# Kernel tuning notes

Hardware: AMD Instinct MI355X
Metric: run time of the kernel (lower is better)

## Reference

```python
import jax, jax.numpy as jnp
import numpy as np

B, T, D, A = 16, 2048, 512, 64


def setup_inputs() -> dict:
    key = jax.random.key(0)
    ks = jax.random.split(key, 7)
    s = 1.0 / np.sqrt(D)
    return {
        "inp": jax.random.normal(ks[0], (B, T, D), dtype=jnp.float32),
        "Wq": jax.random.normal(ks[1], (D, A), dtype=jnp.float32) * s,
        "bq": jax.random.normal(ks[2], (A,), dtype=jnp.float32) * 0.01,
        "Wk": jax.random.normal(ks[3], (D, A), dtype=jnp.float32) * s,
        "bk": jax.random.normal(ks[4], (A,), dtype=jnp.float32) * 0.01,
        "Wv": jax.random.normal(ks[5], (D, A), dtype=jnp.float32) * s,
        "bv": jax.random.normal(ks[6], (A,), dtype=jnp.float32) * 0.01,
    }


def reference(inp, Wq, bq, Wk, bk, Wv, bv):
    # Projections: (B,T,D) @ (D,A) -> (B,T,A)
    Q = inp @ Wq + bq
    K = inp @ Wk + bk
    V = inp @ Wv + bv
    # Scaled QK^T: (B,T,T)
    scores = jnp.einsum("btd,bsd->bts", Q, K) / jnp.sqrt(jnp.float32(A))
    # Sign-based K padding mask: mask[b, s] = sign(|sum_a K[b,s,a]|)
    k_mask = jnp.sign(jnp.abs(K.sum(axis=-1)))  # (B,T)
    scores = jnp.where(k_mask[:, None, :] == 0, jnp.float32(1e-8), scores)
    att = jax.nn.softmax(scores, axis=-1)
    # Sign-based Q mask broadcast along the key axis (faithful to Mask module)
    q_mask = jnp.sign(jnp.abs(Q.sum(axis=-1)))  # (B,T)
    att = att * q_mask[:, None, :]
    # dropout_keep_prob == 1 -> dropout is identity
    ctx = jnp.einsum("bts,bsa->bta", att, V)  # (B,T,A)
    # inp^T @ ctx -> (B,D,A), then sum over A -> (B,D)
    out = jnp.einsum("btd,bta->bd", inp, ctx)
    return out
```

## Files before the change

kernel.cpp:

```cpp
#include <hip/hip_runtime.h>

#define B_ 16
#define T_ 2048
#define D_ 512
#define SCALE_LOG2E 0.18033688f

typedef __bf16 bf16x8 __attribute__((ext_vector_type(8)));
typedef float  f32x4  __attribute__((ext_vector_type(4)));

__device__ inline unsigned short f2bf(float f){
    union { float f; unsigned u; } x; x.f = f;
    unsigned r = x.u + 0x7fffu + ((x.u >> 16) & 1u);
    return (unsigned short)(r >> 16);
}

__device__ inline bf16x8 ldfrag(const unsigned short* p){
    uint4 v = *reinterpret_cast<const uint4*>(p);
    return __builtin_bit_cast(bf16x8, v);
}


__global__ void setup_kernel(const float* __restrict__ Wq, const float* __restrict__ Wk,
                             const float* __restrict__ Wv, const float* __restrict__ bq,
                             const float* __restrict__ bk, const float* __restrict__ bv,
                             unsigned short* __restrict__ WcT, float* __restrict__ bsum,
                             float* __restrict__ numden, float* __restrict__ out)
{
    int e = blockIdx.x * 256 + threadIdx.x;
    if (e < 73728){
        int j = e >> 9, d = e & 511;
        float v;
        if (j < 64)       v = Wq[d * 64 + j];
        else if (j < 128) v = Wk[d * 64 + (j - 64)];
        else if (j < 131){
            const float* src = (j == 128) ? Wq : (j == 129) ? Wk : Wv;
            const float4* p = reinterpret_cast<const float4*>(&src[d * 64]);
            v = 0.f;
            #pragma unroll
            for (int i = 0; i < 16; i++){ float4 t = p[i]; v += (t.x + t.y) + (t.z + t.w); }
        }
        else v = 0.f;
        WcT[j * 512 + d] = f2bf(v);
    } else if (e < 73744){
        int mm = e - 73728;
        float s = 0.f;
        const float* src = (mm == 0) ? bq : (mm == 1) ? bk : bv;
        if (mm < 3){
            const float4* p = reinterpret_cast<const float4*>(src);
            #pragma unroll
            for (int i = 0; i < 16; i++){ float4 t = p[i]; s += (t.x + t.y) + (t.z + t.w); }
        }
        bsum[mm] = s;
    } else if (e < 139280){
        numden[e - 73744] = 0.f;
    } else if (e < 147472){
        out[e - 139280] = 0.f;
    }
}

__global__ __launch_bounds__(256) void proj_kernel(
    const float* __restrict__ inp, const unsigned short* __restrict__ WcT,
    const float* __restrict__ bq, const float* __restrict__ bk,
    const float* __restrict__ bsum,
    unsigned short* __restrict__ Qb, unsigned short* __restrict__ Kb,
    float* __restrict__ wvp)
{
    __shared__ __align__(16) unsigned short Af[4 * 512];
    __shared__ __align__(16) unsigned short Bf[9 * 512];
    const int tid  = threadIdx.x;
    const int r0   = blockIdx.x * 64;
    const int lane = tid & 63, wvid = tid >> 6;
    const int m = lane & 15, q = lane >> 4;

    const int ar = tid >> 2, aseg = tid & 3;
    unsigned short* a_dst = &Af[(ar >> 4) * 512 + (aseg * 16 + (ar & 15)) * 8];
    const float* a_src = &inp[(size_t)(r0 + ar) * 512 + aseg * 8];
    const unsigned short* b_src0 = &WcT[(((tid      ) >> 6) * 16 + (tid & 15)) * 512 + ((tid >> 4) & 3) * 8];
    const unsigned short* b_src1 = &WcT[(((tid + 256) >> 6) * 16 + (tid & 15)) * 512 + ((tid >> 4) & 3) * 8];
    const unsigned short* b_src2 = &WcT[(((tid + 512) >> 6) * 16 + (tid & 15)) * 512 + ((tid >> 4) & 3) * 8];
    uint4* b_dst0 = reinterpret_cast<uint4*>(&Bf[(tid      ) * 8]);
    uint4* b_dst1 = reinterpret_cast<uint4*>(&Bf[(tid + 256) * 8]);
    uint4* b_dst2 = reinterpret_cast<uint4*>(&Bf[(tid + 512) * 8]);

    f32x4 acc[9];
    #pragma unroll
    for (int t = 0; t < 9; t++) acc[t] = (f32x4){0.f, 0.f, 0.f, 0.f};

    float4 ga0 = *reinterpret_cast<const float4*>(a_src);
    float4 ga1 = *reinterpret_cast<const float4*>(a_src + 4);
    uint4 gb0 = *reinterpret_cast<const uint4*>(b_src0);
    uint4 gb1 = *reinterpret_cast<const uint4*>(b_src1);
    uint4 gb2 = (tid < 64) ? *reinterpret_cast<const uint4*>(b_src2) : (uint4){0,0,0,0};

    for (int kk = 0; kk < 512; kk += 32){
        uint4 pk;
        pk.x = f2bf(ga0.x) | ((unsigned)f2bf(ga0.y) << 16);
        pk.y = f2bf(ga0.z) | ((unsigned)f2bf(ga0.w) << 16);
        pk.z = f2bf(ga1.x) | ((unsigned)f2bf(ga1.y) << 16);
        pk.w = f2bf(ga1.z) | ((unsigned)f2bf(ga1.w) << 16);
        *reinterpret_cast<uint4*>(a_dst) = pk;
        *b_dst0 = gb0;
        *b_dst1 = gb1;
        if (tid < 64) *b_dst2 = gb2;
        __syncthreads();
        if (kk < 480){
            ga0 = *reinterpret_cast<const float4*>(a_src + kk + 32);
            ga1 = *reinterpret_cast<const float4*>(a_src + kk + 36);
            gb0 = *reinterpret_cast<const uint4*>(b_src0 + kk + 32);
            gb1 = *reinterpret_cast<const uint4*>(b_src1 + kk + 32);
            if (tid < 64) gb2 = *reinterpret_cast<const uint4*>(b_src2 + kk + 32);
        }
        bf16x8 a = ldfrag(&Af[wvid * 512 + lane * 8]);
        #pragma unroll
        for (int t = 0; t < 9; t++){
            bf16x8 bfr = ldfrag(&Bf[t * 512 + lane * 8]);
            acc[t] = __builtin_amdgcn_mfma_f32_16x16x32_bf16(a, bfr, acc[t], 0, 0, 0);
        }
        __syncthreads();
    }

    float bqv[4], bkv[4];
    #pragma unroll
    for (int t = 0; t < 4; t++){ bqv[t] = bq[t * 16 + m]; bkv[t] = bk[t * 16 + m]; }
    const float bs = bsum[m];

    #pragma unroll
    for (int i = 0; i < 4; i++){
        size_t r = (size_t)r0 + 16 * wvid + q * 4 + i;
        float val = acc[8][i] + bs;
        float qsv = __shfl(val, (lane & 48));
        float ksv = __shfl(val, (lane & 48) | 1);
        float vsv = __shfl(val, (lane & 48) | 2);
        float kz  = (ksv == 0.f) ? 0.f : 1.f;
        #pragma unroll
        for (int t = 0; t < 4; t++)
            Qb[r * 64 + t * 16 + m] = f2bf((acc[t][i] + bqv[t]) * SCALE_LOG2E);
        #pragma unroll
        for (int t = 0; t < 4; t++)
            Kb[r * 64 + t * 16 + m] = f2bf((acc[t + 4][i] + bkv[t]) * kz);
        if (m == 0)
            wvp[r] = (qsv == 0.f) ? 0.f : vsv;
    }
}

__global__ __launch_bounds__(512) void attn_kernel(
    const unsigned short* __restrict__ Qb, const unsigned short* __restrict__ Kb,
    const float* __restrict__ wvp, float* __restrict__ num_g, float* __restrict__ den_g)
{
    __shared__ __align__(16) unsigned short Kf[8 * 512];
    const int tid = threadIdx.x;
    const int lane = tid & 63, wvid = tid >> 6;
    const int m = lane & 15, q = lane >> 4;
    const int b  = blockIdx.y;
    const int t0 = blockIdx.x * 256 + wvid * 32;
    const int s0 = blockIdx.z * 512;
    const size_t base = (size_t)b * T_;

    const unsigned short* qp = &Qb[(base + t0 + m) * 64 + q * 8];
    bf16x8 a00 = ldfrag(qp),            a01 = ldfrag(qp + 32);
    bf16x8 a10 = ldfrag(qp + 16 * 64),  a11 = ldfrag(qp + 16 * 64 + 32);

    const unsigned short* ksrc = &Kb[(base + s0 + (wvid >> 1) * 16 + m) * 64 + (wvid & 1) * 32 + q * 8];
    uint4* kdst = reinterpret_cast<uint4*>(&Kf[wvid * 512 + lane * 8]);
    uint4 stg = *reinterpret_cast<const uint4*>(ksrc);

    float num0[4] = {0,0,0,0}, den0[4] = {0,0,0,0};
    float num1[4] = {0,0,0,0}, den1[4] = {0,0,0,0};

    for (int it = 0; it < 8; it++){
        *kdst = stg;
        __syncthreads();
        if (it < 7) stg = *reinterpret_cast<const uint4*>(ksrc + (it + 1) * 64 * 64);
        float w[4];
        #pragma unroll
        for (int st = 0; st < 4; st++) w[st] = wvp[base + s0 + it * 64 + st * 16 + m];
        #pragma unroll
        for (int st = 0; st < 4; st++){
            bf16x8 b0 = ldfrag(&Kf[(st * 2    ) * 512 + lane * 8]);
            bf16x8 b1 = ldfrag(&Kf[(st * 2 + 1) * 512 + lane * 8]);
            f32x4 z0 = (f32x4){0.f,0.f,0.f,0.f};
            z0 = __builtin_amdgcn_mfma_f32_16x16x32_bf16(a00, b0, z0, 0, 0, 0);
            z0 = __builtin_amdgcn_mfma_f32_16x16x32_bf16(a01, b1, z0, 0, 0, 0);
            f32x4 z1 = (f32x4){0.f,0.f,0.f,0.f};
            z1 = __builtin_amdgcn_mfma_f32_16x16x32_bf16(a10, b0, z1, 0, 0, 0);
            z1 = __builtin_amdgcn_mfma_f32_16x16x32_bf16(a11, b1, z1, 0, 0, 0);
            float wst = w[st];
            #pragma unroll
            for (int i = 0; i < 4; i++){
                float e0 = exp2f(z0[i]);
                den0[i] += e0; num0[i] = fmaf(e0, wst, num0[i]);
                float e1 = exp2f(z1[i]);
                den1[i] += e1; num1[i] = fmaf(e1, wst, num1[i]);
            }
        }
        __syncthreads();
    }
    #pragma unroll
    for (int s = 1; s < 16; s <<= 1){
        #pragma unroll
        for (int i = 0; i < 4; i++){
            num0[i] += __shfl_xor(num0[i], s); den0[i] += __shfl_xor(den0[i], s);
            num1[i] += __shfl_xor(num1[i], s); den1[i] += __shfl_xor(den1[i], s);
        }
    }
    if (m == 0){
        #pragma unroll
        for (int i = 0; i < 4; i++){
            atomicAdd(&num_g[base + t0 + q * 4 + i],      num0[i]);
            atomicAdd(&den_g[base + t0 + q * 4 + i],      den0[i]);
            atomicAdd(&num_g[base + t0 + 16 + q * 4 + i], num1[i]);
            atomicAdd(&den_g[base + t0 + 16 + q * 4 + i], den1[i]);
        }
    }
}

__global__ __launch_bounds__(256) void out_kernel(
    const float* __restrict__ inp, const float* __restrict__ num_g,
    const float* __restrict__ den_g, float* __restrict__ out)
{
    __shared__ float csh[32];
    const int tid = threadIdx.x;
    const int b   = blockIdx.y;
    const int t0  = blockIdx.x * 32;
    const size_t base = (size_t)b * T_;
    if (tid < 32) csh[tid] = num_g[base + t0 + tid] / den_g[base + t0 + tid];
    __syncthreads();
    const float2* ip = reinterpret_cast<const float2*>(inp + (base + t0) * 512);
    float a0 = 0.f, a1 = 0.f;
    #pragma unroll 8
    for (int t = 0; t < 32; t++){
        float ct = csh[t];
        float2 v = ip[(size_t)t * 256 + tid];
        a0 = fmaf(v.x, ct, a0);
        a1 = fmaf(v.y, ct, a1);
    }
    atomicAdd(&out[b * 512 + 2 * tid],     a0);
    atomicAdd(&out[b * 512 + 2 * tid + 1], a1);
}

extern "C" void kernel_launch(void* const* d_in, const int* in_sizes, int n_in,
                              void* d_out, int out_size, void* d_ws, size_t ws_size,
                              hipStream_t stream)
{
    const float* inp = (const float*)d_in[0];
    const float* Wq  = (const float*)d_in[1];
    const float* bq  = (const float*)d_in[2];
    const float* Wk  = (const float*)d_in[3];
    const float* bk  = (const float*)d_in[4];
    const float* Wv  = (const float*)d_in[5];
    const float* bv  = (const float*)d_in[6];
    float* out = (float*)d_out;

    char* ws = (char*)d_ws;
    unsigned short* WcT = (unsigned short*)(ws);
    float* bsum         = (float*)(ws + 147456);
    unsigned short* Qb  = (unsigned short*)(ws + 262144);
    unsigned short* Kb  = (unsigned short*)(ws + 4456448);
    float* wvp          = (float*)(ws + 8650752);
    float* num_g        = (float*)(ws + 8781824);
    float* den_g        = (float*)(ws + 8912896);

    setup_kernel<<<577, 256, 0, stream>>>(Wq, Wk, Wv, bq, bk, bv, WcT, bsum, num_g, out);
    proj_kernel<<<512, 256, 0, stream>>>(inp, WcT, bq, bk, bsum, Qb, Kb, wvp);
    attn_kernel<<<dim3(8, 16, 4), 512, 0, stream>>>(Qb, Kb, wvp, num_g, den_g);
    out_kernel<<<dim3(64, 16), 256, 0, stream>>>(inp, num_g, den_g, out);
}
```

Before: 155.4 us.

## Halve proj block rows, split N tiles across waves, vectorize out_kernel loads

The projection kernel now handles 32 rows per block instead of 64 and launches twice as many blocks. The 9 MFMA column tiles are split between wave pairs (5 and 4), and the K-mask is passed between waves through shared memory. This should give more parallelism on the 256-CU device and less per-wave accumulator pressure, at the cost of reloading the weight tiles for twice as many blocks and adding an extra barrier. The out_kernel switches to float4 loads with two row-phases per block, which doubles the atomicAdd count per block.

```diff
diff --git a/kernel.cpp b/kernel.cpp
--- a/kernel.cpp
+++ b/kernel.cpp
@@ -65,16 +65,18 @@
     unsigned short* __restrict__ Qb, unsigned short* __restrict__ Kb,
     float* __restrict__ wvp)
 {
-    __shared__ __align__(16) unsigned short Af[4 * 512];
+    __shared__ __align__(16) unsigned short Af[2 * 512];
     __shared__ __align__(16) unsigned short Bf[9 * 512];
+    __shared__ float kzsh[32];
     const int tid  = threadIdx.x;
-    const int r0   = blockIdx.x * 64;
+    const int r0   = blockIdx.x * 32;
     const int lane = tid & 63, wvid = tid >> 6;
     const int m = lane & 15, q = lane >> 4;
-
-    const int ar = tid >> 2, aseg = tid & 3;
-    unsigned short* a_dst = &Af[(ar >> 4) * 512 + (aseg * 16 + (ar & 15)) * 8];
-    const float* a_src = &inp[(size_t)(r0 + ar) * 512 + aseg * 8];
+    const int mh = wvid >> 1, nh = wvid & 1;
+
+    const int ar = tid >> 3, aseg = tid & 7;
+    unsigned short* a_dst = &Af[(ar >> 4) * 512 + ((aseg >> 1) * 16 + (ar & 15)) * 8 + (aseg & 1) * 4];
+    const float* a_src = &inp[(size_t)(r0 + ar) * 512 + aseg * 4];
     const unsigned short* b_src0 = &WcT[(((tid      ) >> 6) * 16 + (tid & 15)) * 512 + ((tid >> 4) & 3) * 8];
     const unsigned short* b_src1 = &WcT[(((tid + 256) >> 6) * 16 + (tid & 15)) * 512 + ((tid >> 4) & 3) * 8];
     const unsigned short* b_src2 = &WcT[(((tid + 512) >> 6) * 16 + (tid & 15)) * 512 + ((tid >> 4) & 3) * 8];
@@ -82,64 +84,87 @@
     uint4* b_dst1 = reinterpret_cast<uint4*>(&Bf[(tid + 256) * 8]);
     uint4* b_dst2 = reinterpret_cast<uint4*>(&Bf[(tid + 512) * 8]);
 
-    f32x4 acc[9];
+    f32x4 acc[5];
     #pragma unroll
-    for (int t = 0; t < 9; t++) acc[t] = (f32x4){0.f, 0.f, 0.f, 0.f};
-
-    float4 ga0 = *reinterpret_cast<const float4*>(a_src);
-    float4 ga1 = *reinterpret_cast<const float4*>(a_src + 4);
+    for (int t = 0; t < 5; t++) acc[t] = (f32x4){0.f, 0.f, 0.f, 0.f};
+
+    float4 ga = *reinterpret_cast<const float4*>(a_src);
     uint4 gb0 = *reinterpret_cast<const uint4*>(b_src0);
     uint4 gb1 = *reinterpret_cast<const uint4*>(b_src1);
     uint4 gb2 = (tid < 64) ? *reinterpret_cast<const uint4*>(b_src2) : (uint4){0,0,0,0};
 
+    const int ntile = 5 - nh;
+    const int tbase = nh * 5;
+
     for (int kk = 0; kk < 512; kk += 32){
-        uint4 pk;
-        pk.x = f2bf(ga0.x) | ((unsigned)f2bf(ga0.y) << 16);
-        pk.y = f2bf(ga0.z) | ((unsigned)f2bf(ga0.w) << 16);
-        pk.z = f2bf(ga1.x) | ((unsigned)f2bf(ga1.y) << 16);
-        pk.w = f2bf(ga1.z) | ((unsigned)f2bf(ga1.w) << 16);
-        *reinterpret_cast<uint4*>(a_dst) = pk;
+        ushort4 h; h.x = f2bf(ga.x); h.y = f2bf(ga.y); h.z = f2bf(ga.z); h.w = f2bf(ga.w);
+        *reinterpret_cast<ushort4*>(a_dst) = h;
         *b_dst0 = gb0;
         *b_dst1 = gb1;
         if (tid < 64) *b_dst2 = gb2;
         __syncthreads();
         if (kk < 480){
-            ga0 = *reinterpret_cast<const float4*>(a_src + kk + 32);
-            ga1 = *reinterpret_cast<const float4*>(a_src + kk + 36);
+            ga  = *reinterpret_cast<const float4*>(a_src + kk + 32);
             gb0 = *reinterpret_cast<const uint4*>(b_src0 + kk + 32);
             gb1 = *reinterpret_cast<const uint4*>(b_src1 + kk + 32);
             if (tid < 64) gb2 = *reinterpret_cast<const uint4*>(b_src2 + kk + 32);
         }
-        bf16x8 a = ldfrag(&Af[wvid * 512 + lane * 8]);
-        #pragma unroll
-        for (int t = 0; t < 9; t++){
-            bf16x8 bfr = ldfrag(&Bf[t * 512 + lane * 8]);
-            acc[t] = __builtin_amdgcn_mfma_f32_16x16x32_bf16(a, bfr, acc[t], 0, 0, 0);
-        }
-        __syncthreads();
-    }
-
-    float bqv[4], bkv[4];
-    #pragma unroll
-    for (int t = 0; t < 4; t++){ bqv[t] = bq[t * 16 + m]; bkv[t] = bk[t * 16 + m]; }
-    const float bs = bsum[m];
-
-    #pragma unroll
-    for (int i = 0; i < 4; i++){
-        size_t r = (size_t)r0 + 16 * wvid + q * 4 + i;
-        float val = acc[8][i] + bs;
-        float qsv = __shfl(val, (lane & 48));
-        float ksv = __shfl(val, (lane & 48) | 1);
-        float vsv = __shfl(val, (lane & 48) | 2);
-        float kz  = (ksv == 0.f) ? 0.f : 1.f;
-        #pragma unroll
-        for (int t = 0; t < 4; t++)
-            Qb[r * 64 + t * 16 + m] = f2bf((acc[t][i] + bqv[t]) * SCALE_LOG2E);
-        #pragma unroll
-        for (int t = 0; t < 4; t++)
-            Kb[r * 64 + t * 16 + m] = f2bf((acc[t + 4][i] + bkv[t]) * kz);
-        if (m == 0)
-            wvp[r] = (qsv == 0.f) ? 0.f : vsv;
+        bf16x8 a = ldfrag(&Af[mh * 512 + lane * 8]);
+        #pragma unroll
+        for (int t = 0; t < 5; t++){
+            if (t < ntile){
+                bf16x8 bfr = ldfrag(&Bf[(tbase + t) * 512 + lane * 8]);
+                acc[t] = __builtin_amdgcn_mfma_f32_16x16x32_bf16(a, bfr, acc[t], 0, 0, 0);
+            }
+        }
+        __syncthreads();
+    }
+
+    if (nh == 1){
+        const float bs = bsum[m];
+        #pragma unroll
+        for (int i = 0; i < 4; i++){
+            int rl = mh * 16 + q * 4 + i;
+            float val = acc[3][i] + bs;
+            float qsv = __shfl(val, (lane & 48));
+            float ksv = __shfl(val, (lane & 48) | 1);
+            float vsv = __shfl(val, (lane & 48) | 2);
+            if (m == 0){
+                kzsh[rl] = (ksv == 0.f) ? 0.f : 1.f;
+                wvp[(size_t)r0 + rl] = (qsv == 0.f) ? 0.f : vsv;
+            }
+        }
+    }
+    __syncthreads();
+
+    if (nh == 0){
+        float bqv[4];
+        #pragma unroll
+        for (int t = 0; t < 4; t++) bqv[t] = bq[t * 16 + m];
+        const float bkv0 = bk[m];
+        #pragma unroll
+        for (int i = 0; i < 4; i++){
+            int rl = mh * 16 + q * 4 + i;
+            size_t r = (size_t)r0 + rl;
+            float kz = kzsh[rl];
+            #pragma unroll
+            for (int t = 0; t < 4; t++)
+                Qb[r * 64 + t * 16 + m] = f2bf((acc[t][i] + bqv[t]) * SCALE_LOG2E);
+            Kb[r * 64 + m] = f2bf((acc[4][i] + bkv0) * kz);
+        }
+    } else {
+        float bkv[3];
+        #pragma unroll
+        for (int t = 0; t < 3; t++) bkv[t] = bk[16 + t * 16 + m];
+        #pragma unroll
+        for (int i = 0; i < 4; i++){
+            int rl = mh * 16 + q * 4 + i;
+            size_t r = (size_t)r0 + rl;
+            float kz = kzsh[rl];
+            #pragma unroll
+            for (int t = 0; t < 3; t++)
+                Kb[r * 64 + 16 + t * 16 + m] = f2bf((acc[t][i] + bkv[t]) * kz);
+        }
     }
 }
 
@@ -225,17 +250,24 @@
     const size_t base = (size_t)b * T_;
     if (tid < 32) csh[tid] = num_g[base + t0 + tid] / den_g[base + t0 + tid];
     __syncthreads();
-    const float2* ip = reinterpret_cast<const float2*>(inp + (base + t0) * 512);
-    float a0 = 0.f, a1 = 0.f;
-    #pragma unroll 8
-    for (int t = 0; t < 32; t++){
-        float ct = csh[t];
-        float2 v = ip[(size_t)t * 256 + tid];
-        a0 = fmaf(v.x, ct, a0);
-        a1 = fmaf(v.y, ct, a1);
-    }
-    atomicAdd(&out[b * 512 + 2 * tid],     a0);
-    atomicAdd(&out[b * 512 + 2 * tid + 1], a1);
+    const int c = tid & 127;
+    const int p = tid >> 7;
+    const float4* ip = reinterpret_cast<const float4*>(inp + (base + t0) * 512);
+    float4 a = (float4){0.f, 0.f, 0.f, 0.f};
+    #pragma unroll 4
+    for (int t = 0; t < 16; t++){
+        int row = 2 * t + p;
+        float ct = csh[row];
+        float4 v = ip[(size_t)row * 128 + c];
+        a.x = fmaf(v.x, ct, a.x);
+        a.y = fmaf(v.y, ct, a.y);
+        a.z = fmaf(v.z, ct, a.z);
+        a.w = fmaf(v.w, ct, a.w);
+    }
+    atomicAdd(&out[b * 512 + 4 * c + 0], a.x);
+    atomicAdd(&out[b * 512 + 4 * c + 1], a.y);
+    atomicAdd(&out[b * 512 + 4 * c + 2], a.z);
+    atomicAdd(&out[b * 512 + 4 * c + 3], a.w);
 }
 
 extern "C" void kernel_launch(void* const* d_in, const int* in_sizes, int n_in,
@@ -261,7 +293,7 @@
     float* den_g        = (float*)(ws + 8912896);
 
     setup_kernel<<<577, 256, 0, stream>>>(Wq, Wk, Wv, bq, bk, bv, WcT, bsum, num_g, out);
-    proj_kernel<<<512, 256, 0, stream>>>(inp, WcT, bq, bk, bsum, Qb, Kb, wvp);
+    proj_kernel<<<1024, 256, 0, stream>>>(inp, WcT, bq, bk, bsum, Qb, Kb, wvp);
     attn_kernel<<<dim3(8, 16, 4), 512, 0, stream>>>(Qb, Kb, wvp, num_g, den_g);
     out_kernel<<<dim3(64, 16), 256, 0, stream>>>(inp, num_g, den_g, out);
 }
```

After: 176.1 us. 13.4% more time.

## Split projection GEMM across waves by row pair and column half

Applied to the files above, without the earlier changes.

Each wave in the projection kernel now computes two 16-row fragments over half of the nine output column tiles (5 or 4 tiles), instead of one row fragment over all nine. This halves the B-fragment LDS reads per MFMA and reuses each B fragment across two A fragments. Because the K-sum column now lives in a different wave than the Q columns, the key mask is passed through shared memory with an extra barrier. The work split is uneven (5 vs 4 tiles) and the epilogue adds branch and sync overhead.

```diff
diff --git a/kernel.cpp b/kernel.cpp
--- a/kernel.cpp
+++ b/kernel.cpp
@@ -67,10 +67,12 @@
 {
     __shared__ __align__(16) unsigned short Af[4 * 512];
     __shared__ __align__(16) unsigned short Bf[9 * 512];
+    __shared__ float kzsh[64];
     const int tid  = threadIdx.x;
     const int r0   = blockIdx.x * 64;
     const int lane = tid & 63, wvid = tid >> 6;
     const int m = lane & 15, q = lane >> 4;
+    const int mh = wvid >> 1, nh = wvid & 1;
 
     const int ar = tid >> 2, aseg = tid & 3;
     unsigned short* a_dst = &Af[(ar >> 4) * 512 + (aseg * 16 + (ar & 15)) * 8];
@@ -82,15 +84,21 @@
     uint4* b_dst1 = reinterpret_cast<uint4*>(&Bf[(tid + 256) * 8]);
     uint4* b_dst2 = reinterpret_cast<uint4*>(&Bf[(tid + 512) * 8]);
 
-    f32x4 acc[9];
+    f32x4 acc[5][2];
     #pragma unroll
-    for (int t = 0; t < 9; t++) acc[t] = (f32x4){0.f, 0.f, 0.f, 0.f};
+    for (int t = 0; t < 5; t++){
+        acc[t][0] = (f32x4){0.f, 0.f, 0.f, 0.f};
+        acc[t][1] = (f32x4){0.f, 0.f, 0.f, 0.f};
+    }
 
     float4 ga0 = *reinterpret_cast<const float4*>(a_src);
     float4 ga1 = *reinterpret_cast<const float4*>(a_src + 4);
     uint4 gb0 = *reinterpret_cast<const uint4*>(b_src0);
     uint4 gb1 = *reinterpret_cast<const uint4*>(b_src1);
     uint4 gb2 = (tid < 64) ? *reinterpret_cast<const uint4*>(b_src2) : (uint4){0,0,0,0};
+
+    const int ntile = 5 - nh;
+    const int tbase = nh * 5;
 
     for (int kk = 0; kk < 512; kk += 32){
         uint4 pk;
@@ -110,36 +118,73 @@
             gb1 = *reinterpret_cast<const uint4*>(b_src1 + kk + 32);
             if (tid < 64) gb2 = *reinterpret_cast<const uint4*>(b_src2 + kk + 32);
         }
-        bf16x8 a = ldfrag(&Af[wvid * 512 + lane * 8]);
-        #pragma unroll
-        for (int t = 0; t < 9; t++){
-            bf16x8 bfr = ldfrag(&Bf[t * 512 + lane * 8]);
-            acc[t] = __builtin_amdgcn_mfma_f32_16x16x32_bf16(a, bfr, acc[t], 0, 0, 0);
+        bf16x8 a0 = ldfrag(&Af[(mh * 2    ) * 512 + lane * 8]);
+        bf16x8 a1 = ldfrag(&Af[(mh * 2 + 1) * 512 + lane * 8]);
+        #pragma unroll
+        for (int t = 0; t < 5; t++){
+            if (t < ntile){
+                bf16x8 bfr = ldfrag(&Bf[(tbase + t) * 512 + lane * 8]);
+                acc[t][0] = __builtin_amdgcn_mfma_f32_16x16x32_bf16(a0, bfr, acc[t][0], 0, 0, 0);
+                acc[t][1] = __builtin_amdgcn_mfma_f32_16x16x32_bf16(a1, bfr, acc[t][1], 0, 0, 0);
+            }
         }
         __syncthreads();
     }
 
-    float bqv[4], bkv[4];
-    #pragma unroll
-    for (int t = 0; t < 4; t++){ bqv[t] = bq[t * 16 + m]; bkv[t] = bk[t * 16 + m]; }
-    const float bs = bsum[m];
-
-    #pragma unroll
-    for (int i = 0; i < 4; i++){
-        size_t r = (size_t)r0 + 16 * wvid + q * 4 + i;
-        float val = acc[8][i] + bs;
-        float qsv = __shfl(val, (lane & 48));
-        float ksv = __shfl(val, (lane & 48) | 1);
-        float vsv = __shfl(val, (lane & 48) | 2);
-        float kz  = (ksv == 0.f) ? 0.f : 1.f;
-        #pragma unroll
-        for (int t = 0; t < 4; t++)
-            Qb[r * 64 + t * 16 + m] = f2bf((acc[t][i] + bqv[t]) * SCALE_LOG2E);
-        #pragma unroll
-        for (int t = 0; t < 4; t++)
-            Kb[r * 64 + t * 16 + m] = f2bf((acc[t + 4][i] + bkv[t]) * kz);
-        if (m == 0)
-            wvp[r] = (qsv == 0.f) ? 0.f : vsv;
+    if (nh == 1){
+        const float bs = bsum[m];
+        #pragma unroll
+        for (int f = 0; f < 2; f++){
+            #pragma unroll
+            for (int i = 0; i < 4; i++){
+                int rl = mh * 32 + f * 16 + q * 4 + i;
+                float val = acc[3][f][i] + bs;
+                float qsv = __shfl(val, (lane & 48));
+                float ksv = __shfl(val, (lane & 48) | 1);
+                float vsv = __shfl(val, (lane & 48) | 2);
+                if (m == 0){
+                    kzsh[rl] = (ksv == 0.f) ? 0.f : 1.f;
+                    wvp[(size_t)r0 + rl] = (qsv == 0.f) ? 0.f : vsv;
+                }
+            }
+        }
+    }
+    __syncthreads();
+
+    if (nh == 0){
+        float bqv[4];
+        #pragma unroll
+        for (int t = 0; t < 4; t++) bqv[t] = bq[t * 16 + m];
+        const float bkv0 = bk[m];
+        #pragma unroll
+        for (int f = 0; f < 2; f++){
+            #pragma unroll
+            for (int i = 0; i < 4; i++){
+                int rl = mh * 32 + f * 16 + q * 4 + i;
+                size_t r = (size_t)r0 + rl;
+                float kz = kzsh[rl];
+                #pragma unroll
+                for (int t = 0; t < 4; t++)
+                    Qb[r * 64 + t * 16 + m] = f2bf((acc[t][f][i] + bqv[t]) * SCALE_LOG2E);
+                Kb[r * 64 + m] = f2bf((acc[4][f][i] + bkv0) * kz);
+            }
+        }
+    } else {
+        float bkv[3];
+        #pragma unroll
+        for (int t = 0; t < 3; t++) bkv[t] = bk[16 + t * 16 + m];
+        #pragma unroll
+        for (int f = 0; f < 2; f++){
+            #pragma unroll
+            for (int i = 0; i < 4; i++){
+                int rl = mh * 32 + f * 16 + q * 4 + i;
+                size_t r = (size_t)r0 + rl;
+                float kz = kzsh[rl];
+                #pragma unroll
+                for (int t = 0; t < 3; t++)
+                    Kb[r * 64 + 16 + t * 16 + m] = f2bf((acc[t][f][i] + bkv[t]) * kz);
+            }
+        }
     }
 }
 
```

Result: no change. 154.5 us (-0.6%).
